# Kernel tuning notes

Hardware: AMD Instinct MI355X
Metric: run time of the kernel (lower is better)

Reference implementation:

```python
import jax, jax.numpy as jnp
import numpy as np

NUM_USERS = 100000
NUM_ITEMS = 100000
DIM = 128
B = 8192
H = 200
ATTN_HID = 64


def setup_inputs() -> dict:
    key = jax.random.key(0)
    ks = jax.random.split(key, 10)
    user_ids = jax.random.randint(ks[0], (B,), 0, NUM_USERS)
    item_ids = jax.random.randint(ks[1], (B,), 0, NUM_ITEMS)
    user_history = jax.random.randint(ks[2], (B, H), 0, NUM_ITEMS)
    user_table = jax.random.normal(ks[3], (NUM_USERS, DIM), dtype=jnp.float32)
    item_table = jax.random.normal(ks[4], (NUM_ITEMS, DIM), dtype=jnp.float32)
    feature_interaction = jax.random.normal(ks[5], (DIM, DIM), dtype=jnp.float32)
    # attention MLP: Linear(2*DIM, 64) -> ReLU -> Linear(64, 1) -> Sigmoid
    lim1 = 1.0 / np.sqrt(2 * DIM)
    w1 = jax.random.uniform(ks[6], (2 * DIM, ATTN_HID), minval=-lim1, maxval=lim1, dtype=jnp.float32)
    b1 = jax.random.uniform(ks[7], (ATTN_HID,), minval=-lim1, maxval=lim1, dtype=jnp.float32)
    lim2 = 1.0 / np.sqrt(ATTN_HID)
    w2 = jax.random.uniform(ks[8], (ATTN_HID, 1), minval=-lim2, maxval=lim2, dtype=jnp.float32)
    b2 = jax.random.uniform(ks[9], (1,), minval=-lim2, maxval=lim2, dtype=jnp.float32)
    return {
        "user_ids": user_ids,
        "item_ids": item_ids,
        "user_history": user_history,
        "user_table": user_table,
        "item_table": item_table,
        "feature_interaction": feature_interaction,
        "w1": w1,
        "b1": b1,
        "w2": w2,
        "b2": b2,
    }


def reference(user_ids, item_ids, user_history, user_table, item_table,
              feature_interaction, w1, b1, w2, b2):
    user_emb = user_table[user_ids]          # [B, D]
    item_emb = item_table[item_ids]          # [B, D]
    # bilinear interaction: (user_emb @ W) . item_emb, summed over D -> [B, 1]
    interaction = jnp.sum((user_emb @ feature_interaction) * item_emb, axis=1, keepdims=True)
    # attention-weighted history pooling
    history_emb = item_table[user_history]   # [B, H, D]
    u = jnp.broadcast_to(user_emb[:, None, :], history_emb.shape)  # [B, H, D]
    attn_in = jnp.concatenate([u, history_emb], axis=-1)           # [B, H, 2D]
    h = jax.nn.relu(attn_in @ w1 + b1)                             # [B, H, 64]
    attn_w = jax.nn.sigmoid(h @ w2 + b2)                           # [B, H, 1]
    history_repr = jnp.sum(attn_w * history_emb, axis=1)           # [B, D]
    user_out = user_emb + history_repr
    return (user_out, item_emb, interaction)
```

## Files before the change

### kernel.cpp

```cpp
#include <hip/hip_runtime.h>
#include <math.h>

#define NB      8192
#define HLEN    200
#define DIM     128
#define AH      64
#define NITEMS  100000
#define NTILE   13

typedef __attribute__((ext_vector_type(4))) float f32x4;
typedef __attribute__((ext_vector_type(2))) float f32x2;
typedef __attribute__((ext_vector_type(4))) int   i32x4;
typedef __attribute__((ext_vector_type(8))) short bf16x8;

__device__ __forceinline__ unsigned short f2bf(float f) {
  unsigned int u = __float_as_uint(f);
  u += 0x7fffu + ((u >> 16) & 1u);
  return (unsigned short)(u >> 16);
}
__device__ __forceinline__ float bf2f(unsigned short h) {
  return __uint_as_float(((unsigned int)h) << 16);
}
__device__ __forceinline__ long pick64(const i32x4& v, int h) {
  return (long)(unsigned)v[2 * h] | ((long)(unsigned)v[2 * h + 1] << 32);
}

__global__ void convert_kernel(const float* __restrict__ tbl,
                               const float* __restrict__ w1,
                               unsigned char* __restrict__ tbl8,
                               unsigned char* __restrict__ w1f8) {
  const long total4 = (long)NITEMS * DIM / 4;
  const long stride = (long)gridDim.x * blockDim.x;
  const long t0 = (long)blockIdx.x * blockDim.x + threadIdx.x;
  for (long i = t0; i < total4; i += stride) {
    f32x4 v = ((const f32x4*)tbl)[i];
    int p = __builtin_amdgcn_cvt_pk_fp8_f32(v[0], v[1], 0, false);
    p     = __builtin_amdgcn_cvt_pk_fp8_f32(v[2], v[3], p, true);
    ((int*)tbl8)[i] = p;
  }
  if (t0 < 16384) {
    int L = (int)t0;
    int j  = L & 7, gg = (L >> 3) & 3, mm = (L >> 5) & 15;
    int nt = (L >> 9) & 3, s = (L >> 11) & 3, part = (L >> 13) & 1;
    int kg = part * 128 + (s >> 1) * 64 + gg * 16 + (s & 1) * 8 + j;
    int n  = nt * 16 + mm;
    float v = w1[kg * AH + n];
    int p = __builtin_amdgcn_cvt_pk_fp8_f32(v, v, 0, false);
    w1f8[L] = (unsigned char)(p & 0xff);
  }
}

__global__ __launch_bounds__(256)
void main_kernel_fp8(const int* __restrict__ user_ids,
                     const int* __restrict__ user_history,
                     const float* __restrict__ user_table,
                     const unsigned char* __restrict__ tbl8,
                     const unsigned char* __restrict__ w1f8,
                     const float* __restrict__ b1,
                     const float* __restrict__ w2,
                     const float* __restrict__ b2,
                     float* __restrict__ out_user) {
  const int lane = threadIdx.x & 63;
  const int wave = threadIdx.x >> 6;
  const int b = blockIdx.x * 4 + wave;
  const int m = lane & 15;
  const int g = lane >> 4;

  const int uid = __builtin_amdgcn_readfirstlane(user_ids[b]);
  const float* urow = user_table + (long)uid * DIM;
  const int* hrow = user_history + (long)b * HLEN;

  int idxs[NTILE];
#pragma unroll
  for (int t = 0; t < NTILE; ++t) {
    int row = t * 16 + m;
    idxs[t] = (row < HLEN) ? hrow[row] : 0;
  }

  i32x4 uf[2];
#pragma unroll
  for (int kb = 0; kb < 2; ++kb) {
    const float* up = urow + kb * 64 + g * 16;
    f32x4 q0 = *(const f32x4*)(up + 0);
    f32x4 q1 = *(const f32x4*)(up + 4);
    f32x4 q2 = *(const f32x4*)(up + 8);
    f32x4 q3 = *(const f32x4*)(up + 12);
    i32x4 d;
    d[0] = __builtin_amdgcn_cvt_pk_fp8_f32(q0[0], q0[1], 0, false);
    d[0] = __builtin_amdgcn_cvt_pk_fp8_f32(q0[2], q0[3], d[0], true);
    d[1] = __builtin_amdgcn_cvt_pk_fp8_f32(q1[0], q1[1], 0, false);
    d[1] = __builtin_amdgcn_cvt_pk_fp8_f32(q1[2], q1[3], d[1], true);
    d[2] = __builtin_amdgcn_cvt_pk_fp8_f32(q2[0], q2[1], 0, false);
    d[2] = __builtin_amdgcn_cvt_pk_fp8_f32(q2[2], q2[3], d[2], true);
    d[3] = __builtin_amdgcn_cvt_pk_fp8_f32(q3[0], q3[1], 0, false);
    d[3] = __builtin_amdgcn_cvt_pk_fp8_f32(q3[2], q3[3], d[3], true);
    uf[kb] = d;
  }

  const unsigned char* wtop = w1f8;
  const unsigned char* wbot = w1f8 + 8192;

  f32x4 accu[4];
#pragma unroll
  for (int nt = 0; nt < 4; ++nt) accu[nt] = (f32x4){0.f, 0.f, 0.f, 0.f};
#pragma unroll
  for (int s = 0; s < 4; ++s) {
    long a_s = pick64(uf[s >> 1], s & 1);
#pragma unroll
    for (int nt = 0; nt < 4; ++nt) {
      long bf = *(const long*)(wtop + ((s * 4 + nt) * 16 + m) * 32 + g * 8);
      accu[nt] = __builtin_amdgcn_mfma_f32_16x16x32_fp8_fp8(a_s, bf, accu[nt], 0, 0, 0);
    }
  }
  float ubreg[4], w2reg[4];
#pragma unroll
  for (int nt = 0; nt < 4; ++nt) {
    ubreg[nt] = accu[nt][0] + b1[nt * 16 + m];
    w2reg[nt] = w2[nt * 16 + m];
  }
  const float b2v = b2[0];

  long bfr[4][4];
#pragma unroll
  for (int s = 0; s < 4; ++s)
#pragma unroll
    for (int nt = 0; nt < 4; ++nt)
      bfr[s][nt] = *(const long*)(wbot + ((s * 4 + nt) * 16 + m) * 32 + g * 8);

  float arep[32];
#pragma unroll
  for (int c = 0; c < 32; ++c) arep[c] = 0.f;

  i32x4 pa[3][2];
#define LOADT(T, BUF)                                                          \
  {                                                                            \
    const unsigned char* p_ = tbl8 + ((long)idxs[T] << 7) + g * 16;            \
    pa[BUF][0] = *(const i32x4*)p_;                                            \
    pa[BUF][1] = *(const i32x4*)(p_ + 64);                                     \
  }
  LOADT(0, 0)
  LOADT(1, 1)
#pragma unroll
  for (int t = 0; t < NTILE; ++t) {
    if (t + 2 < NTILE) LOADT(t + 2, (t + 2) % 3)
    const int cb = t % 3;

    f32x4 acc[4];
#pragma unroll
    for (int nt = 0; nt < 4; ++nt) acc[nt] = (f32x4){0.f, 0.f, 0.f, 0.f};
#pragma unroll
    for (int s = 0; s < 4; ++s) {
      long a_s = pick64(pa[cb][s >> 1], s & 1);
#pragma unroll
      for (int nt = 0; nt < 4; ++nt)
        acc[nt] = __builtin_amdgcn_mfma_f32_16x16x32_fp8_fp8(a_s, bfr[s][nt], acc[nt], 0, 0, 0);
    }

    float sums[4];
#pragma unroll
    for (int r = 0; r < 4; ++r) {
      float s = 0.f;
#pragma unroll
      for (int nt = 0; nt < 4; ++nt) {
        float h = fmaxf(acc[nt][r] + ubreg[nt], 0.f);
        s = fmaf(h, w2reg[nt], s);
      }
      s += __shfl_xor(s, 1);
      s += __shfl_xor(s, 2);
      s += __shfl_xor(s, 4);
      s += __shfl_xor(s, 8);
      sums[r] = s;
    }
    const int q = m & 3;
    float keep = (q == 0) ? sums[0] : (q == 1) ? sums[1] : (q == 2) ? sums[2] : sums[3];
    float sv = __shfl(keep, ((m >> 2) << 4) | m);
    float attw = 1.f / (1.f + __expf(-(sv + b2v)));
    if (t * 16 + m >= HLEN) attw = 0.f;

#pragma unroll
    for (int kb = 0; kb < 2; ++kb)
#pragma unroll
      for (int d = 0; d < 4; ++d) {
        f32x2 lo = __builtin_amdgcn_cvt_pk_f32_fp8(pa[cb][kb][d], false);
        f32x2 hi = __builtin_amdgcn_cvt_pk_f32_fp8(pa[cb][kb][d], true);
        const int base = kb * 16 + d * 4;
        arep[base + 0] = fmaf(attw, lo[0], arep[base + 0]);
        arep[base + 1] = fmaf(attw, lo[1], arep[base + 1]);
        arep[base + 2] = fmaf(attw, hi[0], arep[base + 2]);
        arep[base + 3] = fmaf(attw, hi[1], arep[base + 3]);
      }
  }
#undef LOADT

#pragma unroll
  for (int c = 0; c < 32; ++c) {
    arep[c] += __shfl_xor(arep[c], 1);
    arep[c] += __shfl_xor(arep[c], 2);
    arep[c] += __shfl_xor(arep[c], 4);
    arep[c] += __shfl_xor(arep[c], 8);
  }
  if (m == 0) {
#pragma unroll
    for (int kb = 0; kb < 2; ++kb)
#pragma unroll
      for (int i4 = 0; i4 < 4; ++i4) {
        const int col = kb * 64 + g * 16 + i4 * 4;
        f32x4 uv = *(const f32x4*)(urow + col);
        f32x4 o;
#pragma unroll
        for (int qq = 0; qq < 4; ++qq) o[qq] = uv[qq] + arep[kb * 16 + i4 * 4 + qq];
        *(f32x4*)(out_user + (long)b * DIM + col) = o;
      }
  }
}

__global__ __launch_bounds__(256)
void main_fallback(const int* __restrict__ user_ids,
                   const int* __restrict__ user_history,
                   const float* __restrict__ user_table,
                   const float* __restrict__ item_table,
                   const float* __restrict__ w1,
                   const float* __restrict__ b1,
                   const float* __restrict__ w2,
                   const float* __restrict__ b2,
                   float* __restrict__ out_user) {
  const int lane = threadIdx.x & 63;
  const int wave = threadIdx.x >> 6;
  const int b = blockIdx.x * 4 + wave;
  const int m = lane & 15, g = lane >> 4;
  const int uid = __builtin_amdgcn_readfirstlane(user_ids[b]);
  const float* urow = user_table + (long)uid * DIM;
  float upj = b1[lane];
#pragma unroll 8
  for (int d = 0; d < DIM; ++d) upj = fmaf(urow[d], w1[d * AH + lane], upj);
  bf16x8 bfr[4][4];
#pragma unroll
  for (int ks = 0; ks < 4; ++ks)
#pragma unroll
    for (int nt = 0; nt < 4; ++nt) {
      bf16x8 bv;
#pragma unroll
      for (int j = 0; j < 8; ++j)
        bv[j] = (short)f2bf(w1[(DIM + ks * 32 + g * 8 + j) * AH + nt * 16 + m]);
      bfr[ks][nt] = bv;
    }
  float ubreg[4], w2reg[4];
#pragma unroll
  for (int nt = 0; nt < 4; ++nt) {
    ubreg[nt] = __shfl(upj, nt * 16 + m);
    w2reg[nt] = w2[nt * 16 + m];
  }
  const float b2v = b2[0];
  float arep[32];
#pragma unroll
  for (int c = 0; c < 32; ++c) arep[c] = 0.f;
  const int* hrow = user_history + (long)b * HLEN;
  for (int t = 0; t < NTILE; ++t) {
    const int row = t * 16 + m;
    const int idx = (row < HLEN) ? hrow[row] : 0;
    bf16x8 a[4];
    const float* rp = item_table + (long)idx * DIM;
#pragma unroll
    for (int ks = 0; ks < 4; ++ks) {
      f32x4 lo = *(const f32x4*)(rp + ks * 32 + g * 8);
      f32x4 hi = *(const f32x4*)(rp + ks * 32 + g * 8 + 4);
      bf16x8 av;
      av[0] = (short)f2bf(lo[0]); av[1] = (short)f2bf(lo[1]);
      av[2] = (short)f2bf(lo[2]); av[3] = (short)f2bf(lo[3]);
      av[4] = (short)f2bf(hi[0]); av[5] = (short)f2bf(hi[1]);
      av[6] = (short)f2bf(hi[2]); av[7] = (short)f2bf(hi[3]);
      a[ks] = av;
    }
    f32x4 acc[4];
#pragma unroll
    for (int nt = 0; nt < 4; ++nt) acc[nt] = (f32x4){0.f, 0.f, 0.f, 0.f};
#pragma unroll
    for (int ks = 0; ks < 4; ++ks)
#pragma unroll
      for (int nt = 0; nt < 4; ++nt)
        acc[nt] = __builtin_amdgcn_mfma_f32_16x16x32_bf16(a[ks], bfr[ks][nt], acc[nt], 0, 0, 0);
    float sums[4];
#pragma unroll
    for (int r = 0; r < 4; ++r) {
      float s = 0.f;
#pragma unroll
      for (int nt = 0; nt < 4; ++nt) {
        float h = fmaxf(acc[nt][r] + ubreg[nt], 0.f);
        s = fmaf(h, w2reg[nt], s);
      }
      s += __shfl_xor(s, 1); s += __shfl_xor(s, 2);
      s += __shfl_xor(s, 4); s += __shfl_xor(s, 8);
      sums[r] = s;
    }
    const int q = m & 3;
    float keep = (q == 0) ? sums[0] : (q == 1) ? sums[1] : (q == 2) ? sums[2] : sums[3];
    float sv = __shfl(keep, ((m >> 2) << 4) | m);
    float attw = 1.f / (1.f + __expf(-(sv + b2v)));
    if (row >= HLEN) attw = 0.f;
#pragma unroll
    for (int ks = 0; ks < 4; ++ks)
#pragma unroll
      for (int j = 0; j < 8; ++j)
        arep[ks * 8 + j] = fmaf(attw, bf2f((unsigned short)a[ks][j]), arep[ks * 8 + j]);
  }
#pragma unroll
  for (int c = 0; c < 32; ++c) {
    arep[c] += __shfl_xor(arep[c], 1);
    arep[c] += __shfl_xor(arep[c], 2);
    arep[c] += __shfl_xor(arep[c], 4);
    arep[c] += __shfl_xor(arep[c], 8);
  }
  if (m == 0) {
#pragma unroll
    for (int ks = 0; ks < 4; ++ks)
#pragma unroll
      for (int j = 0; j < 8; ++j) {
        const int col = ks * 32 + g * 8 + j;
        out_user[(long)b * DIM + col] = urow[col] + arep[ks * 8 + j];
      }
  }
}

__global__ __launch_bounds__(256, 2)
void inter_kernel(const int* __restrict__ user_ids,
                  const int* __restrict__ item_ids,
                  const float* __restrict__ user_table,
                  const float* __restrict__ item_table,
                  const float* __restrict__ fi,
                  float* __restrict__ out_item,
                  float* __restrict__ out_inter) {
  __shared__ unsigned short fitb[DIM * 130];
  __shared__ float u4[4][DIM];
  __shared__ float red[4][4];
  const int t = threadIdx.x;
  for (int i = t; i < DIM * DIM; i += 256) {
    int d = i >> 7, e = i & 127;
    fitb[e * 130 + d] = f2bf(fi[i]);
  }
  const int col = t & 127;
  const int dh = t >> 7;
  const int lane = t & 63;
  const int wv = t >> 6;
  const int b0 = blockIdx.x * 32;
  const unsigned short* fr = &fitb[col * 130 + dh * 64];

  for (int grp = 0; grp < 8; ++grp) {
    __syncthreads();
    for (int i = t; i < 4 * DIM; i += 256) {
      int bi = i >> 7, d = i & 127;
      u4[bi][d] = user_table[(long)user_ids[b0 + grp * 4 + bi] * DIM + d];
    }
    __syncthreads();
    float a0 = 0.f, a1 = 0.f, a2 = 0.f, a3 = 0.f;
#pragma unroll 4
    for (int d = 0; d < 64; d += 4) {
      float f0 = bf2f(fr[d]), f1 = bf2f(fr[d + 1]), f2 = bf2f(fr[d + 2]), f3 = bf2f(fr[d + 3]);
      f32x4 q0 = *(const f32x4*)&u4[0][dh * 64 + d];
      f32x4 q1 = *(const f32x4*)&u4[1][dh * 64 + d];
      f32x4 q2 = *(const f32x4*)&u4[2][dh * 64 + d];
      f32x4 q3 = *(const f32x4*)&u4[3][dh * 64 + d];
      a0 = fmaf(f0, q0[0], a0); a0 = fmaf(f1, q0[1], a0); a0 = fmaf(f2, q0[2], a0); a0 = fmaf(f3, q0[3], a0);
      a1 = fmaf(f0, q1[0], a1); a1 = fmaf(f1, q1[1], a1); a1 = fmaf(f2, q1[2], a1); a1 = fmaf(f3, q1[3], a1);
      a2 = fmaf(f0, q2[0], a2); a2 = fmaf(f1, q2[1], a2); a2 = fmaf(f2, q2[2], a2); a2 = fmaf(f3, q2[3], a2);
      a3 = fmaf(f0, q3[0], a3); a3 = fmaf(f1, q3[1], a3); a3 = fmaf(f2, q3[2], a3); a3 = fmaf(f3, q3[3], a3);
    }
    const int bb = b0 + grp * 4;
    const float vv0 = item_table[(long)item_ids[bb + 0] * DIM + col];
    const float vv1 = item_table[(long)item_ids[bb + 1] * DIM + col];
    const float vv2 = item_table[(long)item_ids[bb + 2] * DIM + col];
    const float vv3 = item_table[(long)item_ids[bb + 3] * DIM + col];
    if (dh == 0) {
      out_item[(long)(bb + 0) * DIM + col] = vv0;
      out_item[(long)(bb + 1) * DIM + col] = vv1;
      out_item[(long)(bb + 2) * DIM + col] = vv2;
      out_item[(long)(bb + 3) * DIM + col] = vv3;
    }
    float p0 = a0 * vv0, p1 = a1 * vv1, p2 = a2 * vv2, p3 = a3 * vv3;
#pragma unroll
    for (int msk = 1; msk <= 32; msk <<= 1) {
      p0 += __shfl_xor(p0, msk);
      p1 += __shfl_xor(p1, msk);
      p2 += __shfl_xor(p2, msk);
      p3 += __shfl_xor(p3, msk);
    }
    if (lane == 0) { red[wv][0] = p0; red[wv][1] = p1; red[wv][2] = p2; red[wv][3] = p3; }
    __syncthreads();
    if (t < 4)
      out_inter[bb + t] = red[0][t] + red[1][t] + red[2][t] + red[3][t];
  }
}

extern "C" void kernel_launch(void* const* d_in, const int* in_sizes, int n_in,
                              void* d_out, int out_size, void* d_ws, size_t ws_size,
                              hipStream_t stream) {
  const int*   user_ids     = (const int*)d_in[0];
  const int*   item_ids     = (const int*)d_in[1];
  const int*   user_history = (const int*)d_in[2];
  const float* user_table   = (const float*)d_in[3];
  const float* item_table   = (const float*)d_in[4];
  const float* fi           = (const float*)d_in[5];
  const float* w1           = (const float*)d_in[6];
  const float* b1           = (const float*)d_in[7];
  const float* w2           = (const float*)d_in[8];
  const float* b2           = (const float*)d_in[9];

  float* out       = (float*)d_out;
  float* out_user  = out;
  float* out_item  = out + (size_t)NB * DIM;
  float* out_inter = out + (size_t)2 * NB * DIM;

  const size_t need = (size_t)NITEMS * DIM + 16384;
  if (ws_size >= need) {
    unsigned char* tbl8 = (unsigned char*)d_ws;
    unsigned char* w1f8 = tbl8 + (size_t)NITEMS * DIM;
    convert_kernel<<<1536, 256, 0, stream>>>(item_table, w1, tbl8, w1f8);
    main_kernel_fp8<<<NB / 4, 256, 0, stream>>>(user_ids, user_history, user_table,
        tbl8, w1f8, b1, w2, b2, out_user);
  } else {
    main_fallback<<<NB / 4, 256, 0, stream>>>(user_ids, user_history, user_table,
        item_table, w1, b1, w2, b2, out_user);
  }
  inter_kernel<<<NB / 32, 256, 0, stream>>>(user_ids, item_ids, user_table, item_table,
        fi, out_item, out_inter);
}
```

Measured before the change: 106.9 us.

## Quantize item table to packed FP4 and fuse interaction into preprocessing kernel

Replaces the per-call FP8 copy of the item table with a 4-bit (E2M1-style) packed copy, decoded back to FP8 in registers with v_perm lookups before the FP8 MFMAs. This halves the bytes written during conversion and read by the history gather. The interaction/item-output kernel is merged into the conversion kernel as extra blocks, which removes one launch and lets the two run concurrently. The catch is a much coarser history embedding (8 magnitude levels), which risks failing accuracy tolerance, plus extra ALU work for decoding.

```diff
diff --git a/kernel.cpp b/kernel.cpp
--- a/kernel.cpp
+++ b/kernel.cpp
@@ -12,49 +12,144 @@
 typedef __attribute__((ext_vector_type(2))) float f32x2;
 typedef __attribute__((ext_vector_type(4))) int   i32x4;
 typedef __attribute__((ext_vector_type(8))) short bf16x8;
+typedef unsigned int uint;
 
 __device__ __forceinline__ unsigned short f2bf(float f) {
-  unsigned int u = __float_as_uint(f);
+  uint u = __float_as_uint(f);
   u += 0x7fffu + ((u >> 16) & 1u);
   return (unsigned short)(u >> 16);
 }
 __device__ __forceinline__ float bf2f(unsigned short h) {
-  return __uint_as_float(((unsigned int)h) << 16);
-}
-__device__ __forceinline__ long pick64(const i32x4& v, int h) {
-  return (long)(unsigned)v[2 * h] | ((long)(unsigned)v[2 * h + 1] << 32);
-}
-
-__global__ void convert_kernel(const float* __restrict__ tbl,
-                               const float* __restrict__ w1,
-                               unsigned char* __restrict__ tbl8,
-                               unsigned char* __restrict__ w1f8) {
-  const long total4 = (long)NITEMS * DIM / 4;
-  const long stride = (long)gridDim.x * blockDim.x;
-  const long t0 = (long)blockIdx.x * blockDim.x + threadIdx.x;
-  for (long i = t0; i < total4; i += stride) {
-    f32x4 v = ((const f32x4*)tbl)[i];
-    int p = __builtin_amdgcn_cvt_pk_fp8_f32(v[0], v[1], 0, false);
-    p     = __builtin_amdgcn_cvt_pk_fp8_f32(v[2], v[3], p, true);
-    ((int*)tbl8)[i] = p;
-  }
-  if (t0 < 16384) {
-    int L = (int)t0;
-    int j  = L & 7, gg = (L >> 3) & 3, mm = (L >> 5) & 15;
-    int nt = (L >> 9) & 3, s = (L >> 11) & 3, part = (L >> 13) & 1;
-    int kg = part * 128 + (s >> 1) * 64 + gg * 16 + (s & 1) * 8 + j;
-    int n  = nt * 16 + mm;
-    float v = w1[kg * AH + n];
-    int p = __builtin_amdgcn_cvt_pk_fp8_f32(v, v, 0, false);
-    w1f8[L] = (unsigned char)(p & 0xff);
-  }
-}
-
+  return __uint_as_float(((uint)h) << 16);
+}
+
+__device__ __forceinline__ uint permlut(uint sel) {
+  uint d;
+  asm("v_perm_b32 %0, %1, %2, %3" : "=v"(d)
+      : "v"(0x44403C38u), "v"(0x34302800u), "v"(sel));
+  return d;
+}
+__device__ __forceinline__ void dec8(uint w, uint& pe, uint& po) {
+  uint mlo = w & 0x07070707u;
+  uint mhi = (w >> 4) & 0x07070707u;
+  uint slo = (w & 0x08080808u) << 4;
+  uint shi = w & 0x80808080u;
+  pe = permlut(mlo) | slo;
+  po = permlut(mhi) | shi;
+}
+__device__ __forceinline__ uint encf4(float v) {
+  float a = fabsf(v) * 2.0f;
+  uint n = 0;
+  n += (a >= 0.25f); n += (a >= 0.75f); n += (a >= 1.25f); n += (a >= 1.75f);
+  n += (a >= 2.5f);  n += (a >= 3.5f);  n += (a >= 5.0f);
+  return n | ((__float_as_uint(v) >> 28) & 8u);
+}
+
+#define INTER_BLKS (NB / 32)
 __global__ __launch_bounds__(256)
-void main_kernel_fp8(const int* __restrict__ user_ids,
+void pre_kernel(const int* __restrict__ user_ids,
+                const int* __restrict__ item_ids,
+                const float* __restrict__ user_table,
+                const float* __restrict__ item_table,
+                const float* __restrict__ fi,
+                const float* __restrict__ w1,
+                unsigned char* __restrict__ tbl4,
+                unsigned char* __restrict__ w1f8,
+                float* __restrict__ out_item,
+                float* __restrict__ out_inter) {
+  const int t = threadIdx.x;
+  if (blockIdx.x < INTER_BLKS) {
+    __shared__ unsigned short fitb[DIM * 130];
+    __shared__ float u4[4][DIM];
+    __shared__ float red[4][4];
+    for (int i = t; i < DIM * DIM; i += 256) {
+      int d = i >> 7, e = i & 127;
+      fitb[e * 130 + d] = f2bf(fi[i]);
+    }
+    const int col = t & 127;
+    const int dh = t >> 7;
+    const int lane = t & 63;
+    const int wv = t >> 6;
+    const int b0 = blockIdx.x * 32;
+    const unsigned short* fr = &fitb[col * 130 + dh * 64];
+    for (int grp = 0; grp < 8; ++grp) {
+      __syncthreads();
+      for (int i = t; i < 4 * DIM; i += 256) {
+        int bi = i >> 7, d = i & 127;
+        u4[bi][d] = user_table[(long)user_ids[b0 + grp * 4 + bi] * DIM + d];
+      }
+      __syncthreads();
+      float a0 = 0.f, a1 = 0.f, a2 = 0.f, a3 = 0.f;
+#pragma unroll 4
+      for (int d = 0; d < 64; d += 4) {
+        float f0 = bf2f(fr[d]), f1 = bf2f(fr[d + 1]), f2 = bf2f(fr[d + 2]), f3 = bf2f(fr[d + 3]);
+        f32x4 q0 = *(const f32x4*)&u4[0][dh * 64 + d];
+        f32x4 q1 = *(const f32x4*)&u4[1][dh * 64 + d];
+        f32x4 q2 = *(const f32x4*)&u4[2][dh * 64 + d];
+        f32x4 q3 = *(const f32x4*)&u4[3][dh * 64 + d];
+        a0 = fmaf(f0, q0[0], a0); a0 = fmaf(f1, q0[1], a0); a0 = fmaf(f2, q0[2], a0); a0 = fmaf(f3, q0[3], a0);
+        a1 = fmaf(f0, q1[0], a1); a1 = fmaf(f1, q1[1], a1); a1 = fmaf(f2, q1[2], a1); a1 = fmaf(f3, q1[3], a1);
+        a2 = fmaf(f0, q2[0], a2); a2 = fmaf(f1, q2[1], a2); a2 = fmaf(f2, q2[2], a2); a2 = fmaf(f3, q2[3], a2);
+        a3 = fmaf(f0, q3[0], a3); a3 = fmaf(f1, q3[1], a3); a3 = fmaf(f2, q3[2], a3); a3 = fmaf(f3, q3[3], a3);
+      }
+      const int bb = b0 + grp * 4;
+      const float vv0 = item_table[(long)item_ids[bb + 0] * DIM + col];
+      const float vv1 = item_table[(long)item_ids[bb + 1] * DIM + col];
+      const float vv2 = item_table[(long)item_ids[bb + 2] * DIM + col];
+      const float vv3 = item_table[(long)item_ids[bb + 3] * DIM + col];
+      if (dh == 0) {
+        out_item[(long)(bb + 0) * DIM + col] = vv0;
+        out_item[(long)(bb + 1) * DIM + col] = vv1;
+        out_item[(long)(bb + 2) * DIM + col] = vv2;
+        out_item[(long)(bb + 3) * DIM + col] = vv3;
+      }
+      float p0 = a0 * vv0, p1 = a1 * vv1, p2 = a2 * vv2, p3 = a3 * vv3;
+#pragma unroll
+      for (int msk = 1; msk <= 32; msk <<= 1) {
+        p0 += __shfl_xor(p0, msk);
+        p1 += __shfl_xor(p1, msk);
+        p2 += __shfl_xor(p2, msk);
+        p3 += __shfl_xor(p3, msk);
+      }
+      if (lane == 0) { red[wv][0] = p0; red[wv][1] = p1; red[wv][2] = p2; red[wv][3] = p3; }
+      __syncthreads();
+      if (t < 4)
+        out_inter[bb + t] = red[0][t] + red[1][t] + red[2][t] + red[3][t];
+    }
+  } else {
+    const int cb = blockIdx.x - INTER_BLKS;
+    const int cgrid = gridDim.x - INTER_BLKS;
+    const long t0 = (long)cb * 256 + t;
+    const long total = (long)NITEMS * DIM / 8;
+    const long stride = (long)cgrid * 256;
+    for (long o = t0; o < total; o += stride) {
+      const float* p = item_table + o * 8;
+      f32x4 x0 = *(const f32x4*)p;
+      f32x4 x1 = *(const f32x4*)(p + 4);
+      uint w = 0;
+      w |= encf4(x0[0]);       w |= encf4(x0[1]) << 4;
+      w |= encf4(x0[2]) << 8;  w |= encf4(x0[3]) << 12;
+      w |= encf4(x1[0]) << 16; w |= encf4(x1[1]) << 20;
+      w |= encf4(x1[2]) << 24; w |= encf4(x1[3]) << 28;
+      ((uint*)tbl4)[o] = w;
+    }
+    if (t0 < 16384) {
+      int L = (int)t0;
+      int j = L & 7, g = (L >> 3) & 3, m = (L >> 5) & 15;
+      int nt = (L >> 9) & 3, s = (L >> 11) & 3, part = (L >> 13) & 1;
+      int kg = part * 128 + g * 32 + s * 8 + (j & 3) * 2 + (j >> 2);
+      float v = w1[kg * AH + nt * 16 + m];
+      int pk = __builtin_amdgcn_cvt_pk_fp8_f32(v, v, 0, false);
+      w1f8[L] = (unsigned char)(pk & 0xff);
+    }
+  }
+}
+
+__global__ __launch_bounds__(256, 4)
+void main_kernel_fp4(const int* __restrict__ user_ids,
                      const int* __restrict__ user_history,
                      const float* __restrict__ user_table,
-                     const unsigned char* __restrict__ tbl8,
+                     const unsigned char* __restrict__ tbl4,
                      const unsigned char* __restrict__ w1f8,
                      const float* __restrict__ b1,
                      const float* __restrict__ w2,
@@ -77,24 +172,15 @@
     idxs[t] = (row < HLEN) ? hrow[row] : 0;
   }
 
-  i32x4 uf[2];
-#pragma unroll
-  for (int kb = 0; kb < 2; ++kb) {
-    const float* up = urow + kb * 64 + g * 16;
-    f32x4 q0 = *(const f32x4*)(up + 0);
-    f32x4 q1 = *(const f32x4*)(up + 4);
-    f32x4 q2 = *(const f32x4*)(up + 8);
-    f32x4 q3 = *(const f32x4*)(up + 12);
-    i32x4 d;
-    d[0] = __builtin_amdgcn_cvt_pk_fp8_f32(q0[0], q0[1], 0, false);
-    d[0] = __builtin_amdgcn_cvt_pk_fp8_f32(q0[2], q0[3], d[0], true);
-    d[1] = __builtin_amdgcn_cvt_pk_fp8_f32(q1[0], q1[1], 0, false);
-    d[1] = __builtin_amdgcn_cvt_pk_fp8_f32(q1[2], q1[3], d[1], true);
-    d[2] = __builtin_amdgcn_cvt_pk_fp8_f32(q2[0], q2[1], 0, false);
-    d[2] = __builtin_amdgcn_cvt_pk_fp8_f32(q2[2], q2[3], d[2], true);
-    d[3] = __builtin_amdgcn_cvt_pk_fp8_f32(q3[0], q3[1], 0, false);
-    d[3] = __builtin_amdgcn_cvt_pk_fp8_f32(q3[2], q3[3], d[3], true);
-    uf[kb] = d;
+  int ufd[8];
+#pragma unroll
+  for (int s = 0; s < 4; ++s) {
+    const float* up = urow + g * 32 + s * 8;
+    int e = __builtin_amdgcn_cvt_pk_fp8_f32(up[0], up[2], 0, false);
+    e     = __builtin_amdgcn_cvt_pk_fp8_f32(up[4], up[6], e, true);
+    int o = __builtin_amdgcn_cvt_pk_fp8_f32(up[1], up[3], 0, false);
+    o     = __builtin_amdgcn_cvt_pk_fp8_f32(up[5], up[7], o, true);
+    ufd[2 * s] = e; ufd[2 * s + 1] = o;
   }
 
   const unsigned char* wtop = w1f8;
@@ -105,10 +191,10 @@
   for (int nt = 0; nt < 4; ++nt) accu[nt] = (f32x4){0.f, 0.f, 0.f, 0.f};
 #pragma unroll
   for (int s = 0; s < 4; ++s) {
-    long a_s = pick64(uf[s >> 1], s & 1);
+    long a_s = (long)(uint)ufd[2 * s] | ((long)(uint)ufd[2 * s + 1] << 32);
 #pragma unroll
     for (int nt = 0; nt < 4; ++nt) {
-      long bf = *(const long*)(wtop + ((s * 4 + nt) * 16 + m) * 32 + g * 8);
+      long bf = *(const long*)(wtop + (((s * 4 + nt) * 16 + m) * 4 + g) * 8);
       accu[nt] = __builtin_amdgcn_mfma_f32_16x16x32_fp8_fp8(a_s, bf, accu[nt], 0, 0, 0);
     }
   }
@@ -125,19 +211,14 @@
   for (int s = 0; s < 4; ++s)
 #pragma unroll
     for (int nt = 0; nt < 4; ++nt)
-      bfr[s][nt] = *(const long*)(wbot + ((s * 4 + nt) * 16 + m) * 32 + g * 8);
+      bfr[s][nt] = *(const long*)(wbot + (((s * 4 + nt) * 16 + m) * 4 + g) * 8);
 
   float arep[32];
 #pragma unroll
   for (int c = 0; c < 32; ++c) arep[c] = 0.f;
 
-  i32x4 pa[3][2];
-#define LOADT(T, BUF)                                                          \
-  {                                                                            \
-    const unsigned char* p_ = tbl8 + ((long)idxs[T] << 7) + g * 16;            \
-    pa[BUF][0] = *(const i32x4*)p_;                                            \
-    pa[BUF][1] = *(const i32x4*)(p_ + 64);                                     \
-  }
+  i32x4 pa[3];
+#define LOADT(T, BUF) pa[BUF] = *(const i32x4*)(tbl4 + ((long)idxs[T] << 6) + g * 16);
   LOADT(0, 0)
   LOADT(1, 1)
 #pragma unroll
@@ -145,12 +226,20 @@
     if (t + 2 < NTILE) LOADT(t + 2, (t + 2) % 3)
     const int cb = t % 3;
 
+    uint p8[8];
+#pragma unroll
+    for (int i = 0; i < 4; ++i) {
+      uint pe, po;
+      dec8((uint)pa[cb][i], pe, po);
+      p8[2 * i] = pe; p8[2 * i + 1] = po;
+    }
+
     f32x4 acc[4];
 #pragma unroll
     for (int nt = 0; nt < 4; ++nt) acc[nt] = (f32x4){0.f, 0.f, 0.f, 0.f};
 #pragma unroll
     for (int s = 0; s < 4; ++s) {
-      long a_s = pick64(pa[cb][s >> 1], s & 1);
+      long a_s = (long)p8[2 * s] | ((long)p8[2 * s + 1] << 32);
 #pragma unroll
       for (int nt = 0; nt < 4; ++nt)
         acc[nt] = __builtin_amdgcn_mfma_f32_16x16x32_fp8_fp8(a_s, bfr[s][nt], acc[nt], 0, 0, 0);
@@ -178,17 +267,15 @@
     if (t * 16 + m >= HLEN) attw = 0.f;
 
 #pragma unroll
-    for (int kb = 0; kb < 2; ++kb)
-#pragma unroll
-      for (int d = 0; d < 4; ++d) {
-        f32x2 lo = __builtin_amdgcn_cvt_pk_f32_fp8(pa[cb][kb][d], false);
-        f32x2 hi = __builtin_amdgcn_cvt_pk_f32_fp8(pa[cb][kb][d], true);
-        const int base = kb * 16 + d * 4;
-        arep[base + 0] = fmaf(attw, lo[0], arep[base + 0]);
-        arep[base + 1] = fmaf(attw, lo[1], arep[base + 1]);
-        arep[base + 2] = fmaf(attw, hi[0], arep[base + 2]);
-        arep[base + 3] = fmaf(attw, hi[1], arep[base + 3]);
-      }
+    for (int i = 0; i < 8; ++i) {
+      f32x2 lo = __builtin_amdgcn_cvt_pk_f32_fp8(p8[i], false);
+      f32x2 hi = __builtin_amdgcn_cvt_pk_f32_fp8(p8[i], true);
+      const int base = i * 4;
+      arep[base + 0] = fmaf(attw, lo[0], arep[base + 0]);
+      arep[base + 1] = fmaf(attw, lo[1], arep[base + 1]);
+      arep[base + 2] = fmaf(attw, hi[0], arep[base + 2]);
+      arep[base + 3] = fmaf(attw, hi[1], arep[base + 3]);
+    }
   }
 #undef LOADT
 
@@ -201,16 +288,19 @@
   }
   if (m == 0) {
 #pragma unroll
-    for (int kb = 0; kb < 2; ++kb)
-#pragma unroll
-      for (int i4 = 0; i4 < 4; ++i4) {
-        const int col = kb * 64 + g * 16 + i4 * 4;
-        f32x4 uv = *(const f32x4*)(urow + col);
-        f32x4 o;
-#pragma unroll
-        for (int qq = 0; qq < 4; ++qq) o[qq] = uv[qq] + arep[kb * 16 + i4 * 4 + qq];
-        *(f32x4*)(out_user + (long)b * DIM + col) = o;
-      }
+    for (int i = 0; i < 4; ++i) {
+      const int colb = g * 32 + i * 8;
+      const float* ar = &arep[i * 8];
+      f32x4 u0 = *(const f32x4*)(urow + colb);
+      f32x4 u1 = *(const f32x4*)(urow + colb + 4);
+      f32x4 o0, o1;
+      o0[0] = u0[0] + ar[0]; o0[1] = u0[1] + ar[4];
+      o0[2] = u0[2] + ar[1]; o0[3] = u0[3] + ar[5];
+      o1[0] = u1[0] + ar[2]; o1[1] = u1[1] + ar[6];
+      o1[2] = u1[2] + ar[3]; o1[3] = u1[3] + ar[7];
+      *(f32x4*)(out_user + (long)b * DIM + colb) = o0;
+      *(f32x4*)(out_user + (long)b * DIM + colb + 4) = o1;
+    }
   }
 }
 
@@ -321,75 +411,6 @@
   }
 }
 
-__global__ __launch_bounds__(256, 2)
-void inter_kernel(const int* __restrict__ user_ids,
-                  const int* __restrict__ item_ids,
-                  const float* __restrict__ user_table,
-                  const float* __restrict__ item_table,
-                  const float* __restrict__ fi,
-                  float* __restrict__ out_item,
-                  float* __restrict__ out_inter) {
-  __shared__ unsigned short fitb[DIM * 130];
-  __shared__ float u4[4][DIM];
-  __shared__ float red[4][4];
-  const int t = threadIdx.x;
-  for (int i = t; i < DIM * DIM; i += 256) {
-    int d = i >> 7, e = i & 127;
-    fitb[e * 130 + d] = f2bf(fi[i]);
-  }
-  const int col = t & 127;
-  const int dh = t >> 7;
-  const int lane = t & 63;
-  const int wv = t >> 6;
-  const int b0 = blockIdx.x * 32;
-  const unsigned short* fr = &fitb[col * 130 + dh * 64];
-
-  for (int grp = 0; grp < 8; ++grp) {
-    __syncthreads();
-    for (int i = t; i < 4 * DIM; i += 256) {
-      int bi = i >> 7, d = i & 127;
-      u4[bi][d] = user_table[(long)user_ids[b0 + grp * 4 + bi] * DIM + d];
-    }
-    __syncthreads();
-    float a0 = 0.f, a1 = 0.f, a2 = 0.f, a3 = 0.f;
-#pragma unroll 4
-    for (int d = 0; d < 64; d += 4) {
-      float f0 = bf2f(fr[d]), f1 = bf2f(fr[d + 1]), f2 = bf2f(fr[d + 2]), f3 = bf2f(fr[d + 3]);
-      f32x4 q0 = *(const f32x4*)&u4[0][dh * 64 + d];
-      f32x4 q1 = *(const f32x4*)&u4[1][dh * 64 + d];
-      f32x4 q2 = *(const f32x4*)&u4[2][dh * 64 + d];
-      f32x4 q3 = *(const f32x4*)&u4[3][dh * 64 + d];
-      a0 = fmaf(f0, q0[0], a0); a0 = fmaf(f1, q0[1], a0); a0 = fmaf(f2, q0[2], a0); a0 = fmaf(f3, q0[3], a0);
-      a1 = fmaf(f0, q1[0], a1); a1 = fmaf(f1, q1[1], a1); a1 = fmaf(f2, q1[2], a1); a1 = fmaf(f3, q1[3], a1);
-      a2 = fmaf(f0, q2[0], a2); a2 = fmaf(f1, q2[1], a2); a2 = fmaf(f2, q2[2], a2); a2 = fmaf(f3, q2[3], a2);
-      a3 = fmaf(f0, q3[0], a3); a3 = fmaf(f1, q3[1], a3); a3 = fmaf(f2, q3[2], a3); a3 = fmaf(f3, q3[3], a3);
-    }
-    const int bb = b0 + grp * 4;
-    const float vv0 = item_table[(long)item_ids[bb + 0] * DIM + col];
-    const float vv1 = item_table[(long)item_ids[bb + 1] * DIM + col];
-    const float vv2 = item_table[(long)item_ids[bb + 2] * DIM + col];
-    const float vv3 = item_table[(long)item_ids[bb + 3] * DIM + col];
-    if (dh == 0) {
-      out_item[(long)(bb + 0) * DIM + col] = vv0;
-      out_item[(long)(bb + 1) * DIM + col] = vv1;
-      out_item[(long)(bb + 2) * DIM + col] = vv2;
-      out_item[(long)(bb + 3) * DIM + col] = vv3;
-    }
-    float p0 = a0 * vv0, p1 = a1 * vv1, p2 = a2 * vv2, p3 = a3 * vv3;
-#pragma unroll
-    for (int msk = 1; msk <= 32; msk <<= 1) {
-      p0 += __shfl_xor(p0, msk);
-      p1 += __shfl_xor(p1, msk);
-      p2 += __shfl_xor(p2, msk);
-      p3 += __shfl_xor(p3, msk);
-    }
-    if (lane == 0) { red[wv][0] = p0; red[wv][1] = p1; red[wv][2] = p2; red[wv][3] = p3; }
-    __syncthreads();
-    if (t < 4)
-      out_inter[bb + t] = red[0][t] + red[1][t] + red[2][t] + red[3][t];
-  }
-}
-
 extern "C" void kernel_launch(void* const* d_in, const int* in_sizes, int n_in,
                               void* d_out, int out_size, void* d_ws, size_t ws_size,
                               hipStream_t stream) {
@@ -409,17 +430,19 @@
   float* out_item  = out + (size_t)NB * DIM;
   float* out_inter = out + (size_t)2 * NB * DIM;
 
-  const size_t need = (size_t)NITEMS * DIM + 16384;
+  const size_t tbl4_bytes = (size_t)NITEMS * DIM / 2;
+  const size_t need = tbl4_bytes + 16384;
   if (ws_size >= need) {
-    unsigned char* tbl8 = (unsigned char*)d_ws;
-    unsigned char* w1f8 = tbl8 + (size_t)NITEMS * DIM;
-    convert_kernel<<<1536, 256, 0, stream>>>(item_table, w1, tbl8, w1f8);
-    main_kernel_fp8<<<NB / 4, 256, 0, stream>>>(user_ids, user_history, user_table,
-        tbl8, w1f8, b1, w2, b2, out_user);
+    unsigned char* tbl4 = (unsigned char*)d_ws;
+    unsigned char* w1f8 = tbl4 + tbl4_bytes;
+    pre_kernel<<<INTER_BLKS + 1024, 256, 0, stream>>>(user_ids, item_ids, user_table,
+        item_table, fi, w1, tbl4, w1f8, out_item, out_inter);
+    main_kernel_fp4<<<NB / 4, 256, 0, stream>>>(user_ids, user_history, user_table,
+        tbl4, w1f8, b1, w2, b2, out_user);
   } else {
     main_fallback<<<NB / 4, 256, 0, stream>>>(user_ids, user_history, user_table,
         item_table, w1, b1, w2, b2, out_user);
-  }
-  inter_kernel<<<NB / 32, 256, 0, stream>>>(user_ids, item_ids, user_table, item_table,
-        fi, out_item, out_inter);
-}
+    pre_kernel<<<INTER_BLKS, 256, 0, stream>>>(user_ids, item_ids, user_table,
+        item_table, fi, w1, nullptr, nullptr, out_item, out_inter);
+  }
+}
```

New measurement: 118.9 us. +11.2%, slower.

## Fuse interaction and fp8 conversion kernels; swap MFMA operands to drop shuffles

Applied to the files above, without the earlier changes.

Merges the fp8 table conversion and the bilinear interaction/item-copy kernel into one launch. Blocks are split by index, so the interaction work overlaps the conversion instead of running as a separate trailing kernel. In the main kernel, W1 becomes the A operand and history rows the B operand, and the user projection plus b1 is folded into the accumulator init. This lets each lane reduce over its own hidden units, replacing the 16-lane shuffle reduction with two xor-shuffles. The history prefetch also deepens from 2 to 3 tiles, at the cost of more registers.

```diff
diff --git a/kernel.cpp b/kernel.cpp
--- a/kernel.cpp
+++ b/kernel.cpp
@@ -7,59 +7,130 @@
 #define AH      64
 #define NITEMS  100000
 #define NTILE   13
+#define INTER_BLKS (NB / 32)
 
 typedef __attribute__((ext_vector_type(4))) float f32x4;
 typedef __attribute__((ext_vector_type(2))) float f32x2;
 typedef __attribute__((ext_vector_type(4))) int   i32x4;
 typedef __attribute__((ext_vector_type(8))) short bf16x8;
+typedef unsigned int uint;
 
 __device__ __forceinline__ unsigned short f2bf(float f) {
-  unsigned int u = __float_as_uint(f);
+  uint u = __float_as_uint(f);
   u += 0x7fffu + ((u >> 16) & 1u);
   return (unsigned short)(u >> 16);
 }
 __device__ __forceinline__ float bf2f(unsigned short h) {
-  return __uint_as_float(((unsigned int)h) << 16);
+  return __uint_as_float(((uint)h) << 16);
 }
 __device__ __forceinline__ long pick64(const i32x4& v, int h) {
   return (long)(unsigned)v[2 * h] | ((long)(unsigned)v[2 * h + 1] << 32);
 }
 
-__global__ void convert_kernel(const float* __restrict__ tbl,
-                               const float* __restrict__ w1,
-                               unsigned char* __restrict__ tbl8,
-                               unsigned char* __restrict__ w1f8) {
-  const long total4 = (long)NITEMS * DIM / 4;
-  const long stride = (long)gridDim.x * blockDim.x;
-  const long t0 = (long)blockIdx.x * blockDim.x + threadIdx.x;
-  for (long i = t0; i < total4; i += stride) {
-    f32x4 v = ((const f32x4*)tbl)[i];
-    int p = __builtin_amdgcn_cvt_pk_fp8_f32(v[0], v[1], 0, false);
-    p     = __builtin_amdgcn_cvt_pk_fp8_f32(v[2], v[3], p, true);
-    ((int*)tbl8)[i] = p;
-  }
-  if (t0 < 16384) {
-    int L = (int)t0;
-    int j  = L & 7, gg = (L >> 3) & 3, mm = (L >> 5) & 15;
-    int nt = (L >> 9) & 3, s = (L >> 11) & 3, part = (L >> 13) & 1;
-    int kg = part * 128 + (s >> 1) * 64 + gg * 16 + (s & 1) * 8 + j;
-    int n  = nt * 16 + mm;
-    float v = w1[kg * AH + n];
-    int p = __builtin_amdgcn_cvt_pk_fp8_f32(v, v, 0, false);
-    w1f8[L] = (unsigned char)(p & 0xff);
-  }
-}
-
 __global__ __launch_bounds__(256)
-void main_kernel_fp8(const int* __restrict__ user_ids,
-                     const int* __restrict__ user_history,
-                     const float* __restrict__ user_table,
-                     const unsigned char* __restrict__ tbl8,
-                     const unsigned char* __restrict__ w1f8,
-                     const float* __restrict__ b1,
-                     const float* __restrict__ w2,
-                     const float* __restrict__ b2,
-                     float* __restrict__ out_user) {
+void pre_kernel(const int* __restrict__ user_ids,
+                const int* __restrict__ item_ids,
+                const float* __restrict__ user_table,
+                const float* __restrict__ item_table,
+                const float* __restrict__ fi,
+                const float* __restrict__ w1,
+                unsigned char* __restrict__ tbl8,
+                unsigned char* __restrict__ w1a8,
+                float* __restrict__ out_item,
+                float* __restrict__ out_inter) {
+  const int t = threadIdx.x;
+  if (blockIdx.x < INTER_BLKS) {
+    __shared__ unsigned short fitb[DIM * 130];
+    __shared__ float u4[4][DIM];
+    __shared__ float red[4][4];
+    for (int i = t; i < DIM * DIM; i += 256) {
+      int d = i >> 7, e = i & 127;
+      fitb[e * 130 + d] = f2bf(fi[i]);
+    }
+    const int col = t & 127;
+    const int dh = t >> 7;
+    const int lane = t & 63;
+    const int wv = t >> 6;
+    const int b0 = blockIdx.x * 32;
+    const unsigned short* fr = &fitb[col * 130 + dh * 64];
+    for (int grp = 0; grp < 8; ++grp) {
+      __syncthreads();
+      for (int i = t; i < 4 * DIM; i += 256) {
+        int bi = i >> 7, d = i & 127;
+        u4[bi][d] = user_table[(long)user_ids[b0 + grp * 4 + bi] * DIM + d];
+      }
+      __syncthreads();
+      float a0 = 0.f, a1 = 0.f, a2 = 0.f, a3 = 0.f;
+#pragma unroll 4
+      for (int d = 0; d < 64; d += 4) {
+        float f0 = bf2f(fr[d]), f1 = bf2f(fr[d + 1]), f2 = bf2f(fr[d + 2]), f3 = bf2f(fr[d + 3]);
+        f32x4 q0 = *(const f32x4*)&u4[0][dh * 64 + d];
+        f32x4 q1 = *(const f32x4*)&u4[1][dh * 64 + d];
+        f32x4 q2 = *(const f32x4*)&u4[2][dh * 64 + d];
+        f32x4 q3 = *(const f32x4*)&u4[3][dh * 64 + d];
+        a0 = fmaf(f0, q0[0], a0); a0 = fmaf(f1, q0[1], a0); a0 = fmaf(f2, q0[2], a0); a0 = fmaf(f3, q0[3], a0);
+        a1 = fmaf(f0, q1[0], a1); a1 = fmaf(f1, q1[1], a1); a1 = fmaf(f2, q1[2], a1); a1 = fmaf(f3, q1[3], a1);
+        a2 = fmaf(f0, q2[0], a2); a2 = fmaf(f1, q2[1], a2); a2 = fmaf(f2, q2[2], a2); a2 = fmaf(f3, q2[3], a2);
+        a3 = fmaf(f0, q3[0], a3); a3 = fmaf(f1, q3[1], a3); a3 = fmaf(f2, q3[2], a3); a3 = fmaf(f3, q3[3], a3);
+      }
+      const int bb = b0 + grp * 4;
+      const float vv0 = item_table[(long)item_ids[bb + 0] * DIM + col];
+      const float vv1 = item_table[(long)item_ids[bb + 1] * DIM + col];
+      const float vv2 = item_table[(long)item_ids[bb + 2] * DIM + col];
+      const float vv3 = item_table[(long)item_ids[bb + 3] * DIM + col];
+      if (dh == 0) {
+        out_item[(long)(bb + 0) * DIM + col] = vv0;
+        out_item[(long)(bb + 1) * DIM + col] = vv1;
+        out_item[(long)(bb + 2) * DIM + col] = vv2;
+        out_item[(long)(bb + 3) * DIM + col] = vv3;
+      }
+      float p0 = a0 * vv0, p1 = a1 * vv1, p2 = a2 * vv2, p3 = a3 * vv3;
+#pragma unroll
+      for (int msk = 1; msk <= 32; msk <<= 1) {
+        p0 += __shfl_xor(p0, msk);
+        p1 += __shfl_xor(p1, msk);
+        p2 += __shfl_xor(p2, msk);
+        p3 += __shfl_xor(p3, msk);
+      }
+      if (lane == 0) { red[wv][0] = p0; red[wv][1] = p1; red[wv][2] = p2; red[wv][3] = p3; }
+      __syncthreads();
+      if (t < 4)
+        out_inter[bb + t] = red[0][t] + red[1][t] + red[2][t] + red[3][t];
+    }
+  } else {
+    const int cb = blockIdx.x - INTER_BLKS;
+    const int cgrid = gridDim.x - INTER_BLKS;
+    const long t0 = (long)cb * 256 + t;
+    const long total4 = (long)NITEMS * DIM / 4;
+    const long stride = (long)cgrid * 256;
+    for (long i = t0; i < total4; i += stride) {
+      f32x4 v = ((const f32x4*)item_table)[i];
+      int p = __builtin_amdgcn_cvt_pk_fp8_f32(v[0], v[1], 0, false);
+      p     = __builtin_amdgcn_cvt_pk_fp8_f32(v[2], v[3], p, true);
+      ((int*)tbl8)[i] = p;
+    }
+    if (t0 < 16384) {
+      int L = (int)t0;
+      int j = L & 7, g = (L >> 3) & 3, m = (L >> 5) & 15;
+      int nt = (L >> 9) & 3, s = (L >> 11) & 3, part = (L >> 13) & 1;
+      int dim = (s >> 1) * 64 + g * 16 + (s & 1) * 8 + j;
+      float v = w1[(part * 128 + dim) * AH + nt * 16 + m];
+      int pk = __builtin_amdgcn_cvt_pk_fp8_f32(v, v, 0, false);
+      w1a8[L] = (unsigned char)(pk & 0xff);
+    }
+  }
+}
+
+__global__ __launch_bounds__(256)
+void main_kernel_fp8s(const int* __restrict__ user_ids,
+                      const int* __restrict__ user_history,
+                      const float* __restrict__ user_table,
+                      const unsigned char* __restrict__ tbl8,
+                      const unsigned char* __restrict__ w1a8,
+                      const float* __restrict__ b1,
+                      const float* __restrict__ w2,
+                      const float* __restrict__ b2,
+                      float* __restrict__ out_user) {
   const int lane = threadIdx.x & 63;
   const int wave = threadIdx.x >> 6;
   const int b = blockIdx.x * 4 + wave;
@@ -77,104 +148,91 @@
     idxs[t] = (row < HLEN) ? hrow[row] : 0;
   }
 
-  i32x4 uf[2];
-#pragma unroll
-  for (int kb = 0; kb < 2; ++kb) {
-    const float* up = urow + kb * 64 + g * 16;
-    f32x4 q0 = *(const f32x4*)(up + 0);
-    f32x4 q1 = *(const f32x4*)(up + 4);
-    f32x4 q2 = *(const f32x4*)(up + 8);
-    f32x4 q3 = *(const f32x4*)(up + 12);
-    i32x4 d;
-    d[0] = __builtin_amdgcn_cvt_pk_fp8_f32(q0[0], q0[1], 0, false);
-    d[0] = __builtin_amdgcn_cvt_pk_fp8_f32(q0[2], q0[3], d[0], true);
-    d[1] = __builtin_amdgcn_cvt_pk_fp8_f32(q1[0], q1[1], 0, false);
-    d[1] = __builtin_amdgcn_cvt_pk_fp8_f32(q1[2], q1[3], d[1], true);
-    d[2] = __builtin_amdgcn_cvt_pk_fp8_f32(q2[0], q2[1], 0, false);
-    d[2] = __builtin_amdgcn_cvt_pk_fp8_f32(q2[2], q2[3], d[2], true);
-    d[3] = __builtin_amdgcn_cvt_pk_fp8_f32(q3[0], q3[1], 0, false);
-    d[3] = __builtin_amdgcn_cvt_pk_fp8_f32(q3[2], q3[3], d[3], true);
-    uf[kb] = d;
-  }
-
-  const unsigned char* wtop = w1f8;
-  const unsigned char* wbot = w1f8 + 8192;
-
-  f32x4 accu[4];
-#pragma unroll
-  for (int nt = 0; nt < 4; ++nt) accu[nt] = (f32x4){0.f, 0.f, 0.f, 0.f};
-#pragma unroll
-  for (int s = 0; s < 4; ++s) {
-    long a_s = pick64(uf[s >> 1], s & 1);
-#pragma unroll
-    for (int nt = 0; nt < 4; ++nt) {
-      long bf = *(const long*)(wtop + ((s * 4 + nt) * 16 + m) * 32 + g * 8);
-      accu[nt] = __builtin_amdgcn_mfma_f32_16x16x32_fp8_fp8(a_s, bf, accu[nt], 0, 0, 0);
-    }
-  }
-  float ubreg[4], w2reg[4];
-#pragma unroll
-  for (int nt = 0; nt < 4; ++nt) {
-    ubreg[nt] = accu[nt][0] + b1[nt * 16 + m];
-    w2reg[nt] = w2[nt * 16 + m];
-  }
-  const float b2v = b2[0];
-
-  long bfr[4][4];
-#pragma unroll
-  for (int s = 0; s < 4; ++s)
-#pragma unroll
-    for (int nt = 0; nt < 4; ++nt)
-      bfr[s][nt] = *(const long*)(wbot + ((s * 4 + nt) * 16 + m) * 32 + g * 8);
-
-  float arep[32];
-#pragma unroll
-  for (int c = 0; c < 32; ++c) arep[c] = 0.f;
-
-  i32x4 pa[3][2];
+  i32x4 pa[4][2];
 #define LOADT(T, BUF)                                                          \
   {                                                                            \
     const unsigned char* p_ = tbl8 + ((long)idxs[T] << 7) + g * 16;            \
     pa[BUF][0] = *(const i32x4*)p_;                                            \
     pa[BUF][1] = *(const i32x4*)(p_ + 64);                                     \
   }
-  LOADT(0, 0)
-  LOADT(1, 1)
+  LOADT(0, 0) LOADT(1, 1) LOADT(2, 2)
+
+  long ufr[4];
+#pragma unroll
+  for (int s = 0; s < 4; ++s) {
+    const float* up = urow + (s >> 1) * 64 + g * 16 + (s & 1) * 8;
+    f32x4 qa = *(const f32x4*)up;
+    f32x4 qb = *(const f32x4*)(up + 4);
+    int d0 = __builtin_amdgcn_cvt_pk_fp8_f32(qa[0], qa[1], 0, false);
+    d0     = __builtin_amdgcn_cvt_pk_fp8_f32(qa[2], qa[3], d0, true);
+    int d1 = __builtin_amdgcn_cvt_pk_fp8_f32(qb[0], qb[1], 0, false);
+    d1     = __builtin_amdgcn_cvt_pk_fp8_f32(qb[2], qb[3], d1, true);
+    ufr[s] = (long)(uint)d0 | ((long)(uint)d1 << 32);
+  }
+
+  f32x4 accu[4];
+#pragma unroll
+  for (int nt = 0; nt < 4; ++nt) accu[nt] = (f32x4){0.f, 0.f, 0.f, 0.f};
+#pragma unroll
+  for (int s = 0; s < 4; ++s) {
+#pragma unroll
+    for (int nt = 0; nt < 4; ++nt) {
+      long wa = *(const long*)(w1a8 + ((s * 4 + nt) * 16 + m) * 32 + g * 8);
+      accu[nt] = __builtin_amdgcn_mfma_f32_16x16x32_fp8_fp8(wa, ufr[s], accu[nt], 0, 0, 0);
+    }
+  }
+  float ub2[4][4], w2v[4][4];
+#pragma unroll
+  for (int nt = 0; nt < 4; ++nt)
+#pragma unroll
+    for (int r = 0; r < 4; ++r) {
+      const int ah = nt * 16 + g * 4 + r;
+      ub2[nt][r] = accu[nt][r] + b1[ah];
+      w2v[nt][r] = w2[ah];
+    }
+  const float b2v = b2[0];
+
+  long wb[4][4];
+#pragma unroll
+  for (int s = 0; s < 4; ++s)
+#pragma unroll
+    for (int nt = 0; nt < 4; ++nt)
+      wb[s][nt] = *(const long*)(w1a8 + 8192 + ((s * 4 + nt) * 16 + m) * 32 + g * 8);
+
+  float arep[32];
+#pragma unroll
+  for (int c = 0; c < 32; ++c) arep[c] = 0.f;
+
 #pragma unroll
   for (int t = 0; t < NTILE; ++t) {
-    if (t + 2 < NTILE) LOADT(t + 2, (t + 2) % 3)
-    const int cb = t % 3;
+    if (t + 3 < NTILE) LOADT(t + 3, (t + 3) & 3)
+    const int cb = t & 3;
 
     f32x4 acc[4];
 #pragma unroll
-    for (int nt = 0; nt < 4; ++nt) acc[nt] = (f32x4){0.f, 0.f, 0.f, 0.f};
+    for (int nt = 0; nt < 4; ++nt)
+      acc[nt] = (f32x4){ub2[nt][0], ub2[nt][1], ub2[nt][2], ub2[nt][3]};
 #pragma unroll
     for (int s = 0; s < 4; ++s) {
-      long a_s = pick64(pa[cb][s >> 1], s & 1);
+      long bs = pick64(pa[cb][s >> 1], s & 1);
 #pragma unroll
       for (int nt = 0; nt < 4; ++nt)
-        acc[nt] = __builtin_amdgcn_mfma_f32_16x16x32_fp8_fp8(a_s, bfr[s][nt], acc[nt], 0, 0, 0);
-    }
-
-    float sums[4];
-#pragma unroll
-    for (int r = 0; r < 4; ++r) {
-      float s = 0.f;
-#pragma unroll
-      for (int nt = 0; nt < 4; ++nt) {
-        float h = fmaxf(acc[nt][r] + ubreg[nt], 0.f);
-        s = fmaf(h, w2reg[nt], s);
-      }
-      s += __shfl_xor(s, 1);
-      s += __shfl_xor(s, 2);
-      s += __shfl_xor(s, 4);
-      s += __shfl_xor(s, 8);
-      sums[r] = s;
-    }
-    const int q = m & 3;
-    float keep = (q == 0) ? sums[0] : (q == 1) ? sums[1] : (q == 2) ? sums[2] : sums[3];
-    float sv = __shfl(keep, ((m >> 2) << 4) | m);
-    float attw = 1.f / (1.f + __expf(-(sv + b2v)));
+        acc[nt] = __builtin_amdgcn_mfma_f32_16x16x32_fp8_fp8(wb[s][nt], bs, acc[nt], 0, 0, 0);
+    }
+
+    float cn[4];
+#pragma unroll
+    for (int nt = 0; nt < 4; ++nt) {
+      float c = fmaxf(acc[nt][0], 0.f) * w2v[nt][0];
+      c = fmaf(fmaxf(acc[nt][1], 0.f), w2v[nt][1], c);
+      c = fmaf(fmaxf(acc[nt][2], 0.f), w2v[nt][2], c);
+      c = fmaf(fmaxf(acc[nt][3], 0.f), w2v[nt][3], c);
+      cn[nt] = c;
+    }
+    float sl = (cn[0] + cn[1]) + (cn[2] + cn[3]);
+    sl += __shfl_xor(sl, 16);
+    sl += __shfl_xor(sl, 32);
+    float attw = 1.f / (1.f + __expf(-(sl + b2v)));
     if (t * 16 + m >= HLEN) attw = 0.f;
 
 #pragma unroll
@@ -321,75 +379,6 @@
   }
 }
 
-__global__ __launch_bounds__(256, 2)
-void inter_kernel(const int* __restrict__ user_ids,
-                  const int* __restrict__ item_ids,
-                  const float* __restrict__ user_table,
-                  const float* __restrict__ item_table,
-                  const float* __restrict__ fi,
-                  float* __restrict__ out_item,
-                  float* __restrict__ out_inter) {
-  __shared__ unsigned short fitb[DIM * 130];
-  __shared__ float u4[4][DIM];
-  __shared__ float red[4][4];
-  const int t = threadIdx.x;
-  for (int i = t; i < DIM * DIM; i += 256) {
-    int d = i >> 7, e = i & 127;
-    fitb[e * 130 + d] = f2bf(fi[i]);
-  }
-  const int col = t & 127;
-  const int dh = t >> 7;
-  const int lane = t & 63;
-  const int wv = t >> 6;
-  const int b0 = blockIdx.x * 32;
-  const unsigned short* fr = &fitb[col * 130 + dh * 64];
-
-  for (int grp = 0; grp < 8; ++grp) {
-    __syncthreads();
-    for (int i = t; i < 4 * DIM; i += 256) {
-      int bi = i >> 7, d = i & 127;
-      u4[bi][d] = user_table[(long)user_ids[b0 + grp * 4 + bi] * DIM + d];
-    }
-    __syncthreads();
-    float a0 = 0.f, a1 = 0.f, a2 = 0.f, a3 = 0.f;
-#pragma unroll 4
-    for (int d = 0; d < 64; d += 4) {
-      float f0 = bf2f(fr[d]), f1 = bf2f(fr[d + 1]), f2 = bf2f(fr[d + 2]), f3 = bf2f(fr[d + 3]);
-      f32x4 q0 = *(const f32x4*)&u4[0][dh * 64 + d];
-      f32x4 q1 = *(const f32x4*)&u4[1][dh * 64 + d];
-      f32x4 q2 = *(const f32x4*)&u4[2][dh * 64 + d];
-      f32x4 q3 = *(const f32x4*)&u4[3][dh * 64 + d];
-      a0 = fmaf(f0, q0[0], a0); a0 = fmaf(f1, q0[1], a0); a0 = fmaf(f2, q0[2], a0); a0 = fmaf(f3, q0[3], a0);
-      a1 = fmaf(f0, q1[0], a1); a1 = fmaf(f1, q1[1], a1); a1 = fmaf(f2, q1[2], a1); a1 = fmaf(f3, q1[3], a1);
-      a2 = fmaf(f0, q2[0], a2); a2 = fmaf(f1, q2[1], a2); a2 = fmaf(f2, q2[2], a2); a2 = fmaf(f3, q2[3], a2);
-      a3 = fmaf(f0, q3[0], a3); a3 = fmaf(f1, q3[1], a3); a3 = fmaf(f2, q3[2], a3); a3 = fmaf(f3, q3[3], a3);
-    }
-    const int bb = b0 + grp * 4;
-    const float vv0 = item_table[(long)item_ids[bb + 0] * DIM + col];
-    const float vv1 = item_table[(long)item_ids[bb + 1] * DIM + col];
-    const float vv2 = item_table[(long)item_ids[bb + 2] * DIM + col];
-    const float vv3 = item_table[(long)item_ids[bb + 3] * DIM + col];
-    if (dh == 0) {
-      out_item[(long)(bb + 0) * DIM + col] = vv0;
-      out_item[(long)(bb + 1) * DIM + col] = vv1;
-      out_item[(long)(bb + 2) * DIM + col] = vv2;
-      out_item[(long)(bb + 3) * DIM + col] = vv3;
-    }
-    float p0 = a0 * vv0, p1 = a1 * vv1, p2 = a2 * vv2, p3 = a3 * vv3;
-#pragma unroll
-    for (int msk = 1; msk <= 32; msk <<= 1) {
-      p0 += __shfl_xor(p0, msk);
-      p1 += __shfl_xor(p1, msk);
-      p2 += __shfl_xor(p2, msk);
-      p3 += __shfl_xor(p3, msk);
-    }
-    if (lane == 0) { red[wv][0] = p0; red[wv][1] = p1; red[wv][2] = p2; red[wv][3] = p3; }
-    __syncthreads();
-    if (t < 4)
-      out_inter[bb + t] = red[0][t] + red[1][t] + red[2][t] + red[3][t];
-  }
-}
-
 extern "C" void kernel_launch(void* const* d_in, const int* in_sizes, int n_in,
                               void* d_out, int out_size, void* d_ws, size_t ws_size,
                               hipStream_t stream) {
@@ -412,14 +401,15 @@
   const size_t need = (size_t)NITEMS * DIM + 16384;
   if (ws_size >= need) {
     unsigned char* tbl8 = (unsigned char*)d_ws;
-    unsigned char* w1f8 = tbl8 + (size_t)NITEMS * DIM;
-    convert_kernel<<<1536, 256, 0, stream>>>(item_table, w1, tbl8, w1f8);
-    main_kernel_fp8<<<NB / 4, 256, 0, stream>>>(user_ids, user_history, user_table,
-        tbl8, w1f8, b1, w2, b2, out_user);
+    unsigned char* w1a8 = tbl8 + (size_t)NITEMS * DIM;
+    pre_kernel<<<INTER_BLKS + 1024, 256, 0, stream>>>(user_ids, item_ids, user_table,
+        item_table, fi, w1, tbl8, w1a8, out_item, out_inter);
+    main_kernel_fp8s<<<NB / 4, 256, 0, stream>>>(user_ids, user_history, user_table,
+        tbl8, w1a8, b1, w2, b2, out_user);
   } else {
     main_fallback<<<NB / 4, 256, 0, stream>>>(user_ids, user_history, user_table,
         item_table, w1, b1, w2, b2, out_user);
-  }
-  inter_kernel<<<NB / 32, 256, 0, stream>>>(user_ids, item_ids, user_table, item_table,
-        fi, out_item, out_inter);
-}
+    pre_kernel<<<INTER_BLKS, 256, 0, stream>>>(user_ids, item_ids, user_table,
+        item_table, fi, w1, nullptr, nullptr, out_item, out_inter);
+  }
+}
```

Result: slower. 127.3 us (+19.0%).
